# Optimization experiments

Hardware: AMD Instinct MI355X
Metric: run time of the kernel (lower is better)

The kernel has to match this reference:

```python
import jax, jax.numpy as jnp
import numpy as np
from jax import lax

NUM_CLASSES = 80
INPUT_SIZE = 416.0
CONF_THR = 0.5
IOU_THR = 0.5
# Standard YOLOv3 COCO anchors; anchors[3*idx:3*idx+3] pairs large anchors with 13x13 head.
ANCHORS = np.array([[116, 90], [156, 198], [373, 326],
                    [30, 61], [62, 45], [59, 119],
                    [10, 13], [16, 30], [33, 23]], dtype=np.float32)


def setup_inputs() -> dict:
    key = jax.random.key(0)
    k0, k1, k2 = jax.random.split(key, 3)
    C = 3 * (5 + NUM_CLASSES)  # 255
    return {
        "p0": jax.random.normal(k0, (1, C, 13, 13), dtype=jnp.float32),
        "p1": jax.random.normal(k1, (1, C, 26, 26), dtype=jnp.float32),
        "p2": jax.random.normal(k2, (1, C, 52, 52), dtype=jnp.float32),
    }


def _decode(pred, anchors):
    # pred: [B, na*(5+nc), H, W]; anchors: [na, 2] in input_size scale
    b, _, lh, lw = pred.shape
    na = anchors.shape[0]
    stride_w = INPUT_SIZE / lw
    stride_h = INPUT_SIZE / lh
    scaled_anchors = anchors / jnp.array([stride_w, stride_h], dtype=pred.dtype)  # [na,2]
    p = pred.reshape(b, na, 5 + NUM_CLASSES, lh, lw).transpose(0, 1, 3, 4, 2)  # [b,na,h,w,ch]
    gx, gy = jnp.meshgrid(jnp.arange(lw, dtype=pred.dtype),
                          jnp.arange(lh, dtype=pred.dtype), indexing='xy')
    grid = jnp.stack([gx, gy], axis=-1)  # [h,w,2], grid[h,w]=(w,h)
    pxy = jax.nn.sigmoid(p[..., 0:2]) + grid  # broadcast over b,na
    pwh = jnp.exp(p[..., 2:4]) * scaled_anchors[None, :, None, None, :]
    stride = jnp.array([stride_w, stride_h, stride_w, stride_h], dtype=pred.dtype)
    pbox = jnp.concatenate([pxy, pwh], axis=-1).reshape(b, -1, 4) * stride
    pconf = jax.nn.sigmoid(p[..., 4]).reshape(b, -1)
    # argmax over sigmoid(logits) == argmax over logits (monotonic)
    pcls = jnp.argmax(p[..., 5:], axis=-1).reshape(b, -1)
    return pbox, pconf, pcls


def _nms(boxes, conf, cls):
    # boxes: [N,4] (cx,cy,w,h), conf: [N], cls: [N] int
    N = boxes.shape[0]
    valid = conf >= CONF_THR
    score = jnp.where(valid, conf, -1.0)
    order = jnp.argsort(-score)  # descending confidence, invalid at the end
    b = boxes[order]
    v = valid[order]
    c = cls[order]
    s = conf[order]
    # corners
    half = b[:, 2:4] * 0.5
    x1y1 = b[:, 0:2] - half
    x2y2 = b[:, 0:2] + half
    area = b[:, 2] * b[:, 3]
    # pairwise IoU [N,N] (dominant, memory-bound intermediate)
    lt = jnp.maximum(x1y1[:, None, :], x1y1[None, :, :])
    rb = jnp.minimum(x2y2[:, None, :], x2y2[None, :, :])
    wh = jnp.clip(rb - lt, 0.0)
    inter = wh[..., 0] * wh[..., 1]
    union = area[:, None] + area[None, :] - inter
    iou = inter / jnp.maximum(union, 1e-9)
    same_cls = c[:, None] == c[None, :]
    sup_cand = same_cls & (iou > IOU_THR)  # candidate suppressors
    idx = jnp.arange(N)

    def body(i, keep):
        suppressed = jnp.any(keep & (idx < i) & sup_cand[i])
        return keep.at[i].set(v[i] & jnp.logical_not(suppressed))

    keep = lax.fori_loop(0, N, body, jnp.zeros((N,), dtype=bool))
    out = jnp.concatenate([b, s[:, None], c.astype(b.dtype)[:, None]], axis=-1)
    return jnp.where(keep[:, None], out, 0.0)


def reference(p0, p1, p2):
    preds = [p0, p1, p2]
    boxes, confs, clss = [], [], []
    for i, p in enumerate(preds):
        anc = jnp.asarray(ANCHORS[3 * i:3 * i + 3])
        pb, pc, pk = _decode(p, anc)
        boxes.append(pb)
        confs.append(pc)
        clss.append(pk)
    boxes = jnp.concatenate(boxes, axis=1)[0]   # [10647,4]
    conf = jnp.concatenate(confs, axis=1)[0]    # [10647]
    cls = jnp.concatenate(clss, axis=1)[0]      # [10647]
    return _nms(boxes, conf, cls)
```

## Files before the change

### kernel.cpp

```cpp
#include <hip/hip_runtime.h>
#include <stdint.h>

#define N_TOT 10647
#define NB    42
#define NBD   167
#define NCLS  80
#define BCAP  320
#define WPB   5

typedef unsigned long long ull;

#define G_CNT  0
#define G_V    NCLS

__constant__ float c_aw[9] = {116.f,156.f,373.f, 30.f,62.f,59.f, 10.f,16.f,33.f};
__constant__ float c_ah[9] = { 90.f,198.f,326.f, 61.f,45.f,119.f, 13.f,30.f,23.f};

__device__ __forceinline__ float sigmoidf_(float x) { return 1.0f / (1.0f + expf(-x)); }

__global__ void __launch_bounds__(256)
decode_kernel(const float* __restrict__ p0, const float* __restrict__ p1,
              const float* __restrict__ p2,
              float* __restrict__ box, float* __restrict__ conf,
              float* __restrict__ score, int* __restrict__ cls,
              int* __restrict__ rank, int* __restrict__ gctr)
{
    __shared__ float sbest[4][64];
    __shared__ int   sbi[4][64];
    if (blockIdx.x == 0 && threadIdx.x <= NCLS) gctr[threadIdx.x] = 0;
    int sub  = threadIdx.x >> 6;
    int lane = threadIdx.x & 63;
    int n = blockIdx.x * 64 + lane;
    bool inb = (n < N_TOT);
    const float* p; int H, base, lvl; float stride;
    int nn = inb ? n : 0;
    if (nn < 507)       { p = p0; H = 13; base = 0;    stride = 32.f; lvl = 0; }
    else if (nn < 2535) { p = p1; H = 26; base = 507;  stride = 16.f; lvl = 1; }
    else                { p = p2; H = 52; base = 2535; stride = 8.f;  lvl = 2; }
    int m   = nn - base;
    int HW  = H * H;
    int a   = m / HW;
    int rem = m - a * HW;
    const float* q = p + (size_t)(a * 85) * HW + rem;
    float best = -3.4e38f; int bi = 20 * sub;
    if (inb) {
        int c0 = 20 * sub;
        #pragma unroll 5
        for (int c = c0; c < c0 + 20; ++c) {
            float v = q[(size_t)(5 + c) * HW];
            if (v > best) { best = v; bi = c; }
        }
    }
    sbest[sub][lane] = best;
    sbi[sub][lane]   = bi;
    __syncthreads();
    if (sub == 0 && inb) {
        rank[n] = 0;
        float b0 = sbest[0][lane]; int i0 = sbi[0][lane];
        #pragma unroll
        for (int s = 1; s < 4; ++s) {
            float bs = sbest[s][lane];
            if (bs > b0) { b0 = bs; i0 = sbi[s][lane]; }
        }
        int gy = rem / H;
        int gx = rem - gy * H;
        float tx = q[0];
        float ty = q[(size_t)HW];
        float tw = q[(size_t)2*HW];
        float th = q[(size_t)3*HW];
        float tc = q[(size_t)4*HW];
        float cx = (sigmoidf_(tx) + (float)gx) * stride;
        float cy = (sigmoidf_(ty) + (float)gy) * stride;
        float bw = expf(tw) * c_aw[lvl*3 + a];
        float bh = expf(th) * c_ah[lvl*3 + a];
        float cf = sigmoidf_(tc);
        box[n*4+0] = cx; box[n*4+1] = cy; box[n*4+2] = bw; box[n*4+3] = bh;
        conf[n] = cf;
        cls[n]  = i0;
        score[n] = (cf >= 0.5f) ? cf : -1.0f;
    }
}

__global__ void __launch_bounds__(256)
rank_bucket_kernel(const float* __restrict__ score, const float* __restrict__ box,
                   const float* __restrict__ conf, const int* __restrict__ cls,
                   int* __restrict__ rank, int* __restrict__ gctr,
                   float4* __restrict__ cbox4, float* __restrict__ cconf,
                   int* __restrict__ cidx)
{
    __shared__ float tile[256];
    __shared__ int s_cnt;
    const int tid = threadIdx.x;
    if (blockIdx.y < NB) {
        int i   = blockIdx.x * 256 + tid;
        int j0  = blockIdx.y * 256;
        int jj  = j0 + tid;
        tile[tid] = (jj < N_TOT) ? score[jj] : -2.0f;
        __syncthreads();
        float si = (i < N_TOT) ? score[i] : -2.0f;
        if (i >= N_TOT || si < 0.0f) return;
        int r = 0;
        #pragma unroll 8
        for (int t = 0; t < 256; ++t) {
            float sj = tile[t];
            r += (sj > si || (sj == si && (j0 + t) < i)) ? 1 : 0;
        }
        if (r) atomicAdd(&rank[i], r);
    } else {
        if (tid == 0) s_cnt = 0;
        __syncthreads();
        int i = blockIdx.x * 256 + tid;
        if (i < N_TOT && score[i] >= 0.0f) {
            int c = cls[i];
            int pos = atomicAdd(&gctr[G_CNT + c], 1);
            if (pos < BCAP) {
                cbox4[c * BCAP + pos] = *(const float4*)&box[i * 4];
                cconf[c * BCAP + pos] = conf[i];
                cidx[c * BCAP + pos]  = i;
            }
            atomicAdd(&s_cnt, 1);
        }
        __syncthreads();
        if (tid == 0 && s_cnt) atomicAdd(&gctr[G_V], s_cnt);
    }
}

__global__ void __launch_bounds__(256)
class_nms_kernel(const float4* __restrict__ cbox4, const float* __restrict__ cconf,
                 const int* __restrict__ cidx, const int* __restrict__ rank,
                 const int* __restrict__ gctr, float* __restrict__ out)
{
    __shared__ float bcx[BCAP], bcy[BCAP], bw_[BCAP], bh_[BCAP], bcf[BCAP];
    __shared__ uint16_t brank[BCAP];
    __shared__ ull smask[BCAP][WPB];
    __shared__ ull keepm[WPB], nxtm[WPB];
    __shared__ int s_changed;
    const int c   = blockIdx.x;
    const int tid = threadIdx.x;
    const int n   = min(gctr[G_CNT + c], BCAP);
    const int V   = gctr[G_V];
    for (int a = tid; a < n; a += 256) {
        float4 b4 = cbox4[c * BCAP + a];
        bcx[a] = b4.x; bcy[a] = b4.y; bw_[a] = b4.z; bh_[a] = b4.w;
        bcf[a] = cconf[c * BCAP + a];
        brank[a] = (uint16_t)rank[cidx[c * BCAP + a]];
    }
    __syncthreads();
    for (int a = tid; a < n; a += 256) {
        float ax1 = bcx[a] - bw_[a]*0.5f, ay1 = bcy[a] - bh_[a]*0.5f;
        float ax2 = bcx[a] + bw_[a]*0.5f, ay2 = bcy[a] + bh_[a]*0.5f;
        float aar = bw_[a] * bh_[a];
        int ra = brank[a];
        ull msk[WPB] = {0,0,0,0,0};
        for (int b = 0; b < n; ++b) {
            if (b == a) continue;
            if (brank[b] >= ra) continue;
            float bx1 = bcx[b] - bw_[b]*0.5f, by1 = bcy[b] - bh_[b]*0.5f;
            float bx2 = bcx[b] + bw_[b]*0.5f, by2 = bcy[b] + bh_[b]*0.5f;
            float xx1 = fmaxf(ax1, bx1);
            float yy1 = fmaxf(ay1, by1);
            float xx2 = fminf(ax2, bx2);
            float yy2 = fminf(ay2, by2);
            float w = fmaxf(xx2 - xx1, 0.0f);
            float h = fmaxf(yy2 - yy1, 0.0f);
            float inter = w * h;
            float uni   = aar + bw_[b]*bh_[b] - inter;
            float iou   = inter / fmaxf(uni, 1e-9f);
            if (iou > 0.5f) msk[b >> 6] |= (1ull << (b & 63));
        }
        #pragma unroll
        for (int w = 0; w < WPB; ++w) smask[a][w] = msk[w];
    }
    if (tid < WPB) {
        int rem = n - (tid << 6);
        keepm[tid] = (rem >= 64) ? ~0ull : ((rem > 0) ? ((1ull << rem) - 1ull) : 0ull);
    }
    __syncthreads();
    for (int round = 0; round <= n + 2 && n > 0; ++round) {
        if (tid < WPB) nxtm[tid] = 0ull;
        if (tid == 0) s_changed = 0;
        __syncthreads();
        for (int a = tid; a < n; a += 256) {
            ull sup = 0ull;
            #pragma unroll
            for (int w = 0; w < WPB; ++w) sup |= (smask[a][w] & keepm[w]);
            if (sup == 0ull) atomicOr(&nxtm[a >> 6], 1ull << (a & 63));
        }
        __syncthreads();
        if (tid < WPB) {
            if (nxtm[tid] != keepm[tid]) { s_changed = 1; keepm[tid] = nxtm[tid]; }
        }
        __syncthreads();
        if (!s_changed) break;
        __syncthreads();
    }
    for (int a = tid; a < n; a += 256) {
        int r = brank[a];
        bool kept = (keepm[a >> 6] >> (a & 63)) & 1ull;
        float v0=0.f,v1=0.f,v2=0.f,v3=0.f,v4=0.f,v5=0.f;
        if (kept) {
            v0 = bcx[a]; v1 = bcy[a]; v2 = bw_[a]; v3 = bh_[a];
            v4 = bcf[a]; v5 = (float)c;
        }
        out[r*6+0]=v0; out[r*6+1]=v1; out[r*6+2]=v2;
        out[r*6+3]=v3; out[r*6+4]=v4; out[r*6+5]=v5;
    }
    int tail  = N_TOT - V;
    int chunk = (tail + NCLS - 1) / NCLS;
    int rbeg  = V + c * chunk;
    int rend  = min(rbeg + chunk, N_TOT);
    for (int r = rbeg + tid; r < rend; r += 256) {
        out[r*6+0]=0.f; out[r*6+1]=0.f; out[r*6+2]=0.f;
        out[r*6+3]=0.f; out[r*6+4]=0.f; out[r*6+5]=0.f;
    }
}

extern "C" void kernel_launch(void* const* d_in, const int* in_sizes, int n_in,
                              void* d_out, int out_size, void* d_ws, size_t ws_size,
                              hipStream_t stream) {
    const float* p0 = (const float*)d_in[0];
    const float* p1 = (const float*)d_in[1];
    const float* p2 = (const float*)d_in[2];
    float* out = (float*)d_out;
    char* ws = (char*)d_ws;
    const int N = N_TOT;

    float* box   = (float*)ws;
    float* conf  = box + 4*N;
    float* score = conf + N;
    int* cls   = (int*)(score + N);
    int* rank  = cls + N;
    int* gctr  = rank + N;
    float4* cbox4 = (float4*)(((uintptr_t)(gctr + NCLS + 1) + 15) & ~(uintptr_t)15);
    float*  cconf = (float*)(cbox4 + NCLS * BCAP);
    int*    cidx  = (int*)(cconf + NCLS * BCAP);

    decode_kernel<<<NBD, 256, 0, stream>>>(p0, p1, p2, box, conf, score, cls, rank, gctr);
    rank_bucket_kernel<<<dim3(NB, NB + 1), 256, 0, stream>>>(score, box, conf, cls,
                                                             rank, gctr, cbox4, cconf, cidx);
    class_nms_kernel<<<NCLS, 256, 0, stream>>>(cbox4, cconf, cidx, rank, gctr, out);
}
```

Before: 46.91 us.

## Fuse decode, rank and bucketing into one kernel with partial-rank buffer

Merges the decode and the rank/bucket kernels into a single launch. Rank blocks recompute confidence scores directly from the raw predictions, so they no longer depend on decode output. Rank blocks write per-tile partial counts to a 42-slice buffer instead of using atomics, and the NMS kernel sums the slices for each candidate. Decode now computes box values only for boxes above threshold and buckets them inline, and the counters are cleared with a memset. This removes one launch and the intermediate box/conf/score/cls arrays, at the cost of a memset call and 42 gathered loads per candidate in NMS.

```diff
diff --git a/kernel.cpp b/kernel.cpp
--- a/kernel.cpp
+++ b/kernel.cpp
@@ -4,6 +4,7 @@
 #define N_TOT 10647
 #define NB    42
 #define NBD   167
+#define NRB   (NB * NB)
 #define NCLS  80
 #define BCAP  320
 #define WPB   5
@@ -18,116 +19,125 @@
 
 __device__ __forceinline__ float sigmoidf_(float x) { return 1.0f / (1.0f + expf(-x)); }
 
+__device__ __forceinline__ float score_of(int n, const float* __restrict__ p0,
+                                          const float* __restrict__ p1,
+                                          const float* __restrict__ p2)
+{
+    float tc;
+    if (n < 507) {
+        int a = n / 169, rem = n - a * 169;
+        tc = p0[(a * 85 + 4) * 169 + rem];
+    } else if (n < 2535) {
+        int m = n - 507;
+        int a = m / 676, rem = m - a * 676;
+        tc = p1[(a * 85 + 4) * 676 + rem];
+    } else {
+        int m = n - 2535;
+        int a = m / 2704, rem = m - a * 2704;
+        tc = p2[(a * 85 + 4) * 2704 + rem];
+    }
+    float cf = sigmoidf_(tc);
+    return (cf >= 0.5f) ? cf : -1.0f;
+}
+
 __global__ void __launch_bounds__(256)
-decode_kernel(const float* __restrict__ p0, const float* __restrict__ p1,
-              const float* __restrict__ p2,
-              float* __restrict__ box, float* __restrict__ conf,
-              float* __restrict__ score, int* __restrict__ cls,
-              int* __restrict__ rank, int* __restrict__ gctr)
+mega_kernel(const float* __restrict__ p0, const float* __restrict__ p1,
+            const float* __restrict__ p2,
+            int* __restrict__ gctr, float4* __restrict__ cbox4,
+            float* __restrict__ cconf, int* __restrict__ cidx,
+            int* __restrict__ rank42)
 {
     __shared__ float sbest[4][64];
     __shared__ int   sbi[4][64];
-    if (blockIdx.x == 0 && threadIdx.x <= NCLS) gctr[threadIdx.x] = 0;
-    int sub  = threadIdx.x >> 6;
-    int lane = threadIdx.x & 63;
-    int n = blockIdx.x * 64 + lane;
-    bool inb = (n < N_TOT);
-    const float* p; int H, base, lvl; float stride;
-    int nn = inb ? n : 0;
-    if (nn < 507)       { p = p0; H = 13; base = 0;    stride = 32.f; lvl = 0; }
-    else if (nn < 2535) { p = p1; H = 26; base = 507;  stride = 16.f; lvl = 1; }
-    else                { p = p2; H = 52; base = 2535; stride = 8.f;  lvl = 2; }
-    int m   = nn - base;
-    int HW  = H * H;
-    int a   = m / HW;
-    int rem = m - a * HW;
-    const float* q = p + (size_t)(a * 85) * HW + rem;
-    float best = -3.4e38f; int bi = 20 * sub;
-    if (inb) {
-        int c0 = 20 * sub;
-        #pragma unroll 5
-        for (int c = c0; c < c0 + 20; ++c) {
-            float v = q[(size_t)(5 + c) * HW];
-            if (v > best) { best = v; bi = c; }
-        }
-    }
-    sbest[sub][lane] = best;
-    sbi[sub][lane]   = bi;
-    __syncthreads();
-    if (sub == 0 && inb) {
-        rank[n] = 0;
-        float b0 = sbest[0][lane]; int i0 = sbi[0][lane];
-        #pragma unroll
-        for (int s = 1; s < 4; ++s) {
-            float bs = sbest[s][lane];
-            if (bs > b0) { b0 = bs; i0 = sbi[s][lane]; }
-        }
-        int gy = rem / H;
-        int gx = rem - gy * H;
-        float tx = q[0];
-        float ty = q[(size_t)HW];
-        float tw = q[(size_t)2*HW];
-        float th = q[(size_t)3*HW];
-        float tc = q[(size_t)4*HW];
-        float cx = (sigmoidf_(tx) + (float)gx) * stride;
-        float cy = (sigmoidf_(ty) + (float)gy) * stride;
-        float bw = expf(tw) * c_aw[lvl*3 + a];
-        float bh = expf(th) * c_ah[lvl*3 + a];
-        float cf = sigmoidf_(tc);
-        box[n*4+0] = cx; box[n*4+1] = cy; box[n*4+2] = bw; box[n*4+3] = bh;
-        conf[n] = cf;
-        cls[n]  = i0;
-        score[n] = (cf >= 0.5f) ? cf : -1.0f;
-    }
-}
-
-__global__ void __launch_bounds__(256)
-rank_bucket_kernel(const float* __restrict__ score, const float* __restrict__ box,
-                   const float* __restrict__ conf, const int* __restrict__ cls,
-                   int* __restrict__ rank, int* __restrict__ gctr,
-                   float4* __restrict__ cbox4, float* __restrict__ cconf,
-                   int* __restrict__ cidx)
-{
     __shared__ float tile[256];
-    __shared__ int s_cnt;
+    __shared__ int   s_cnt;
+    const int bid = blockIdx.x;
     const int tid = threadIdx.x;
-    if (blockIdx.y < NB) {
-        int i   = blockIdx.x * 256 + tid;
-        int j0  = blockIdx.y * 256;
-        int jj  = j0 + tid;
-        tile[tid] = (jj < N_TOT) ? score[jj] : -2.0f;
-        __syncthreads();
-        float si = (i < N_TOT) ? score[i] : -2.0f;
-        if (i >= N_TOT || si < 0.0f) return;
+
+    if (bid < NBD) {
+        if (tid == 0) s_cnt = 0;
+        int sub  = tid >> 6;
+        int lane = tid & 63;
+        int n = bid * 64 + lane;
+        bool inb = (n < N_TOT);
+        const float* p; int H, base, lvl; float stride;
+        int nn = inb ? n : 0;
+        if (nn < 507)       { p = p0; H = 13; base = 0;    stride = 32.f; lvl = 0; }
+        else if (nn < 2535) { p = p1; H = 26; base = 507;  stride = 16.f; lvl = 1; }
+        else                { p = p2; H = 52; base = 2535; stride = 8.f;  lvl = 2; }
+        int m   = nn - base;
+        int HW  = H * H;
+        int a   = m / HW;
+        int rem = m - a * HW;
+        const float* q = p + (size_t)(a * 85) * HW + rem;
+        float best = -3.4e38f; int bi = 20 * sub;
+        if (inb) {
+            int c0 = 20 * sub;
+            #pragma unroll 5
+            for (int c = c0; c < c0 + 20; ++c) {
+                float v = q[(size_t)(5 + c) * HW];
+                if (v > best) { best = v; bi = c; }
+            }
+        }
+        sbest[sub][lane] = best;
+        sbi[sub][lane]   = bi;
+        __syncthreads();
+        if (sub == 0 && inb) {
+            float b0 = sbest[0][lane]; int i0 = sbi[0][lane];
+            #pragma unroll
+            for (int s = 1; s < 4; ++s) {
+                float bs = sbest[s][lane];
+                if (bs > b0) { b0 = bs; i0 = sbi[s][lane]; }
+            }
+            float tc = q[(size_t)4*HW];
+            float cf = sigmoidf_(tc);
+            if (cf >= 0.5f) {
+                int gy = rem / H;
+                int gx = rem - gy * H;
+                float tx = q[0];
+                float ty = q[(size_t)HW];
+                float tw = q[(size_t)2*HW];
+                float th = q[(size_t)3*HW];
+                float cx = (sigmoidf_(tx) + (float)gx) * stride;
+                float cy = (sigmoidf_(ty) + (float)gy) * stride;
+                float bw = expf(tw) * c_aw[lvl*3 + a];
+                float bh = expf(th) * c_ah[lvl*3 + a];
+                int pos = atomicAdd(&gctr[G_CNT + i0], 1);
+                if (pos < BCAP) {
+                    cbox4[i0 * BCAP + pos] = make_float4(cx, cy, bw, bh);
+                    cconf[i0 * BCAP + pos] = cf;
+                    cidx[i0 * BCAP + pos]  = n;
+                }
+                atomicAdd(&s_cnt, 1);
+            }
+        }
+        __syncthreads();
+        if (tid == 0 && s_cnt) atomicAdd(&gctr[G_V], s_cnt);
+    } else {
+        int rb = bid - NBD;
+        int bx = rb / NB;
+        int by = rb - bx * NB;
+        int j0 = by * 256;
+        int jj = j0 + tid;
+        tile[tid] = (jj < N_TOT) ? score_of(jj, p0, p1, p2) : -2.0f;
+        __syncthreads();
+        int i = bx * 256 + tid;
+        if (i >= N_TOT) return;
+        float si = score_of(i, p0, p1, p2);
+        if (si < 0.0f) return;
         int r = 0;
         #pragma unroll 8
         for (int t = 0; t < 256; ++t) {
             float sj = tile[t];
             r += (sj > si || (sj == si && (j0 + t) < i)) ? 1 : 0;
         }
-        if (r) atomicAdd(&rank[i], r);
-    } else {
-        if (tid == 0) s_cnt = 0;
-        __syncthreads();
-        int i = blockIdx.x * 256 + tid;
-        if (i < N_TOT && score[i] >= 0.0f) {
-            int c = cls[i];
-            int pos = atomicAdd(&gctr[G_CNT + c], 1);
-            if (pos < BCAP) {
-                cbox4[c * BCAP + pos] = *(const float4*)&box[i * 4];
-                cconf[c * BCAP + pos] = conf[i];
-                cidx[c * BCAP + pos]  = i;
-            }
-            atomicAdd(&s_cnt, 1);
-        }
-        __syncthreads();
-        if (tid == 0 && s_cnt) atomicAdd(&gctr[G_V], s_cnt);
+        rank42[(size_t)by * N_TOT + i] = r;
     }
 }
 
 __global__ void __launch_bounds__(256)
 class_nms_kernel(const float4* __restrict__ cbox4, const float* __restrict__ cconf,
-                 const int* __restrict__ cidx, const int* __restrict__ rank,
+                 const int* __restrict__ cidx, const int* __restrict__ rank42,
                  const int* __restrict__ gctr, float* __restrict__ out)
 {
     __shared__ float bcx[BCAP], bcy[BCAP], bw_[BCAP], bh_[BCAP], bcf[BCAP];
@@ -143,7 +153,11 @@
         float4 b4 = cbox4[c * BCAP + a];
         bcx[a] = b4.x; bcy[a] = b4.y; bw_[a] = b4.z; bh_[a] = b4.w;
         bcf[a] = cconf[c * BCAP + a];
-        brank[a] = (uint16_t)rank[cidx[c * BCAP + a]];
+        int idx = cidx[c * BCAP + a];
+        int r = 0;
+        #pragma unroll
+        for (int s = 0; s < NB; ++s) r += rank42[(size_t)s * N_TOT + idx];
+        brank[a] = (uint16_t)r;
     }
     __syncthreads();
     for (int a = tid; a < n; a += 256) {
@@ -225,18 +239,14 @@
     char* ws = (char*)d_ws;
     const int N = N_TOT;
 
-    float* box   = (float*)ws;
-    float* conf  = box + 4*N;
-    float* score = conf + N;
-    int* cls   = (int*)(score + N);
-    int* rank  = cls + N;
-    int* gctr  = rank + N;
+    int* gctr = (int*)ws;
     float4* cbox4 = (float4*)(((uintptr_t)(gctr + NCLS + 1) + 15) & ~(uintptr_t)15);
     float*  cconf = (float*)(cbox4 + NCLS * BCAP);
     int*    cidx  = (int*)(cconf + NCLS * BCAP);
-
-    decode_kernel<<<NBD, 256, 0, stream>>>(p0, p1, p2, box, conf, score, cls, rank, gctr);
-    rank_bucket_kernel<<<dim3(NB, NB + 1), 256, 0, stream>>>(score, box, conf, cls,
-                                                             rank, gctr, cbox4, cconf, cidx);
-    class_nms_kernel<<<NCLS, 256, 0, stream>>>(cbox4, cconf, cidx, rank, gctr, out);
-}
+    int*    rank42 = cidx + NCLS * BCAP;
+
+    hipMemsetAsync(gctr, 0, (NCLS + 1) * sizeof(int), stream);
+    mega_kernel<<<NBD + NRB, 256, 0, stream>>>(p0, p1, p2, gctr, cbox4, cconf,
+                                               cidx, rank42);
+    class_nms_kernel<<<NCLS, 256, 0, stream>>>(cbox4, cconf, cidx, rank42, gctr, out);
+}
```

After: 56.84 us. +21.2%, slower.
